# Kernel tuning notes

Measured on AMD Instinct MI355X. Metric: run time of the kernel, lower is better.

The kernel has to match this reference:

```python
import jax, jax.numpy as jnp
import numpy as np

G, N, H = 32, 128, 32
EDGE_ATTR_DIM = 16
NUM_SPATIAL = 512
NUM_EDGE_DIS = 128
MAX_DIST = 5
N_EDGES = 65536
N_PATHS = 1048576
N_LAYERS = 12


def setup_inputs() -> dict:
    key = jax.random.key(0)
    ks = jax.random.split(key, 8)
    rng = np.random.default_rng(0)
    attn_bias = jax.random.normal(ks[0], (G, N + 1, N + 1), jnp.float32)
    spatial_pos = jax.random.randint(ks[1], (G, N, N), 0, NUM_SPATIAL, jnp.int32)
    # unique (g,i,j) edge destinations -> deterministic scatter
    flat_e = rng.permutation(G * N * N)[:N_EDGES]
    g = flat_e // (N * N)
    rest = flat_e % (N * N)
    edge_index = jnp.asarray(np.stack([g, rest // N, rest % N]), jnp.int32)
    edge_attr = jax.random.normal(ks[2], (N_EDGES, EDGE_ATTR_DIM), jnp.float32)
    # unique (g,i,j,d) path destinations
    flat_p = rng.permutation(G * N * N * MAX_DIST)[:N_PATHS]
    pg = flat_p // (N * N * MAX_DIST)
    r = flat_p % (N * N * MAX_DIST)
    pi = r // (N * MAX_DIST)
    r = r % (N * MAX_DIST)
    pj = r // MAX_DIST
    pd = r % MAX_DIST
    src = rng.integers(0, N, N_PATHS)
    dst = rng.integers(0, N, N_PATHS)
    path_index = jnp.asarray(np.stack([pg, pi, pj, pd, src, dst]), jnp.int32)
    std = 0.02 / np.sqrt(N_LAYERS)
    edge_enc_w = jax.random.normal(ks[3], (H, EDGE_ATTR_DIM), jnp.float32) * std
    spatial_pos_emb = (jax.random.normal(ks[4], (NUM_SPATIAL, H), jnp.float32) * 0.02).at[0].set(0.0)  # padding_idx=0
    virt_dist = jax.random.normal(ks[5], (1, H), jnp.float32) * 0.02
    edge_dis_emb = jax.random.normal(ks[6], (NUM_EDGE_DIS * H * H, 1), jnp.float32) * 0.02
    return dict(attn_bias=attn_bias, spatial_pos=spatial_pos, edge_index=edge_index,
                edge_attr=edge_attr, path_index=path_index, edge_enc_w=edge_enc_w,
                spatial_pos_emb=spatial_pos_emb, virt_dist=virt_dist,
                edge_dis_emb=edge_dis_emb, max_dist=MAX_DIST)


def reference(attn_bias, spatial_pos, edge_index, edge_attr, path_index,
              edge_enc_w, spatial_pos_emb, virt_dist, edge_dis_emb, max_dist):
    n_graph, n1, _ = attn_bias.shape
    n_node = n1 - 1
    num_heads = edge_enc_w.shape[0]
    # [G, H, N+1, N+1] base bias (repeat over heads)
    gab = jnp.broadcast_to(attn_bias[:, None], (n_graph, num_heads, n1, n1))
    # spatial position bias: embedding lookup [G,N,N,H] -> [G,H,N,N]
    spb = jnp.transpose(spatial_pos_emb[spatial_pos], (0, 3, 1, 2))
    gab = gab.at[:, :, 1:, 1:].add(spb)
    t = virt_dist.reshape(1, num_heads, 1)
    gab = gab.at[:, :, 1:, 0].add(t)
    gab = gab.at[:, :, 0, :].add(t)
    # edge encoder: [E, edge_attr_dim] @ [edge_attr_dim, H] -> [E, H]
    ea = edge_attr @ edge_enc_w.T
    dense_adj = jnp.zeros((n_graph, n_node, n_node, num_heads), ea.dtype)
    dense_adj = dense_adj.at[edge_index[0], edge_index[1], edge_index[2]].set(ea)
    # multi-hop path features: scatter gathered edges into [G,N,N,D,H]
    edge_input = jnp.zeros((n_graph, n_node, n_node, max_dist, num_heads), ea.dtype)
    gathered = dense_adj[path_index[0], path_index[4], path_index[5]]
    edge_input = edge_input.at[path_index[0], path_index[1], path_index[2], path_index[3]].set(gathered)
    # path length normalizer
    sp = jnp.where(spatial_pos == 0, 1, spatial_pos)
    sp = jnp.where(sp > 1, sp - 1, sp)
    sp = jnp.clip(sp, 0, max_dist)
    # per-distance head mixing: [D, G*N*N, H] x [D, H, H]
    flat = jnp.transpose(edge_input, (3, 0, 1, 2, 4)).reshape(max_dist, -1, num_heads)
    W = edge_dis_emb.reshape(-1, num_heads, num_heads)[:max_dist]
    flat = jnp.einsum('dnh,dhk->dnk', flat, W)
    ei = flat.reshape(max_dist, n_graph, n_node, n_node, num_heads).transpose(1, 2, 3, 0, 4)
    ei = (ei.sum(-2) / sp[..., None].astype(ei.dtype)).transpose(0, 3, 1, 2)
    gab = gab.at[:, :, 1:, 1:].add(ei)
    return gab + attn_bias[:, None]
```

## Files before the change

### kernel.cpp

```cpp
#include <hip/hip_runtime.h>

#define G_    32
#define N_    128
#define NP1_  129
#define H_    32
#define EAD_  16
#define MAXD_ 5
#define NE_   65536
#define NPTH_ 1048576
#define PPB_  1024

__global__ __launch_bounds__(256) void edge_encode_kernel(
    const float* __restrict__ edge_attr,
    const int*   __restrict__ edge_index,
    const float* __restrict__ edge_enc_w,
    float*       __restrict__ eaval,
    int*         __restrict__ edge_map) {
  int t = blockIdx.x * blockDim.x + threadIdx.x;
  if (t >= NE_ * H_) return;
  int e = t >> 5;
  int h = t & 31;
  const float* ea = edge_attr + e * EAD_;
  const float* w  = edge_enc_w + h * EAD_;
  float s = 0.f;
#pragma unroll
  for (int k = 0; k < EAD_; ++k) s += ea[k] * w[k];
  eaval[t] = s;
  if (h == 0) {
    int g = edge_index[e];
    int i = edge_index[NE_ + e];
    int j = edge_index[2 * NE_ + e];
    edge_map[(g * N_ + i) * N_ + j] = e + 1;
  }
}

__global__ __launch_bounds__(256) void path_fused_kernel(
    const int*   __restrict__ path_index,
    const int*   __restrict__ edge_map,
    const float* __restrict__ eaval,
    const float* __restrict__ Wdis,
    float*       __restrict__ acc) {
  __shared__ int q_p[PPB_];
  __shared__ int q_e[PPB_];
  __shared__ int q_cnt;
  int tid = threadIdx.x;
  if (tid == 0) q_cnt = 0;
  __syncthreads();

  int base = blockIdx.x * PPB_;
#pragma unroll
  for (int k = 0; k < PPB_; k += 256) {
    int p = base + k + tid;
    int pg = path_index[p];
    int ps = path_index[4 * NPTH_ + p];
    int pt = path_index[5 * NPTH_ + p];
    int m = edge_map[(pg * N_ + ps) * N_ + pt];
    if (m) {
      int idx = atomicAdd(&q_cnt, 1);
      q_p[idx] = p;
      q_e[idx] = m - 1;
    }
  }
  __syncthreads();
  int cnt = q_cnt;

  int lane = tid & 31;
  int grp  = tid & 32;
  for (int s = tid >> 5; s < cnt; s += 8) {
    int p = q_p[s];
    int e = q_e[s];
    int pg = path_index[p];
    int pi = path_index[NPTH_ + p];
    int pj = path_index[2 * NPTH_ + p];
    int pd = path_index[3 * NPTH_ + p];
    float rv = eaval[e * H_ + lane];
    const float* Wd = Wdis + pd * H_ * H_;
    float v = 0.f;
#pragma unroll
    for (int h = 0; h < H_; ++h) {
      float rh = __shfl(rv, grp + h, 64);
      v += rh * Wd[h * H_ + lane];
    }
    atomicAdd(&acc[(((pg * N_) + pi) * N_ + pj) * H_ + lane], v);
  }
}

__global__ __launch_bounds__(256) void output_kernel(
    const float* __restrict__ attn_bias,
    const int*   __restrict__ spatial_pos,
    const float* __restrict__ spe,
    const float* __restrict__ virt,
    const float* __restrict__ acc,
    float*       __restrict__ out) {
  __shared__ float lds_val[N_ * 33];
  __shared__ float lds_virt[H_];

  int blk = blockIdx.x;
  int g = blk / NP1_;
  int a = blk - g * NP1_;
  int tid = threadIdx.x;

  if (tid < H_) lds_virt[tid] = virt[tid];

  const float* ab = attn_bias + (g * NP1_ + a) * NP1_;

  if (a == 0) {
    __syncthreads();
    for (int t = tid; t < H_ * NP1_; t += 256) {
      int h = t / NP1_;
      int b = t - h * NP1_;
      out[((g * H_ + h) * NP1_) * NP1_ + b] = 2.f * ab[b] + lds_virt[h];
    }
    return;
  }

  int i = a - 1;
  const float* acc_row = acc + ((g * N_ + i) * N_) * H_;
  const int*   sp_row  = spatial_pos + (g * N_ + i) * N_;

  for (int t = tid; t < N_ * H_; t += 256) {
    int j = t >> 5;
    int h = t & 31;
    int s = sp_row[j];
    int s2 = (s == 0) ? 1 : s;
    s2 = (s2 > 1) ? s2 - 1 : s2;
    s2 = (s2 > MAXD_) ? MAXD_ : s2;
    float inv = 1.0f / (float)s2;
    lds_val[j * 33 + h] = spe[s * H_ + h] + acc_row[t] * inv;
  }
  __syncthreads();

  for (int t = tid; t < H_ * NP1_; t += 256) {
    int h = t / NP1_;
    int b = t - h * NP1_;
    float val = 2.f * ab[b];
    if (b == 0) {
      val += lds_virt[h];
    } else {
      val += lds_val[(b - 1) * 33 + h];
    }
    out[((g * H_ + h) * NP1_ + a) * NP1_ + b] = val;
  }
}

extern "C" void kernel_launch(void* const* d_in, const int* in_sizes, int n_in,
                              void* d_out, int out_size, void* d_ws, size_t ws_size,
                              hipStream_t stream) {
  const float* attn_bias   = (const float*)d_in[0];
  const int*   spatial_pos = (const int*)d_in[1];
  const int*   edge_index  = (const int*)d_in[2];
  const float* edge_attr   = (const float*)d_in[3];
  const int*   path_index  = (const int*)d_in[4];
  const float* edge_enc_w  = (const float*)d_in[5];
  const float* spe         = (const float*)d_in[6];
  const float* virt        = (const float*)d_in[7];
  const float* edge_dis    = (const float*)d_in[8];
  float* out = (float*)d_out;

  const size_t ACC_ELEMS = (size_t)G_ * N_ * N_ * H_;
  const size_t MAP_ELEMS = (size_t)G_ * N_ * N_;

  float* acc      = (float*)d_ws;
  int*   edge_map = (int*)(acc + ACC_ELEMS);
  float* eaval    = (float*)(edge_map + MAP_ELEMS);

  hipMemsetAsync(acc, 0, (ACC_ELEMS + MAP_ELEMS) * sizeof(float), stream);

  {
    int total = NE_ * H_;
    edge_encode_kernel<<<(total + 255) / 256, 256, 0, stream>>>(
        edge_attr, edge_index, edge_enc_w, eaval, edge_map);
  }
  path_fused_kernel<<<NPTH_ / PPB_, 256, 0, stream>>>(
      path_index, edge_map, eaval, edge_dis, acc);
  output_kernel<<<G_ * NP1_, 256, 0, stream>>>(
      attn_bias, spatial_pos, spe, virt, acc, out);
}
```

Before: 105.8 us.

## Scatter path edge ids into slot table and fuse head-mixing into output kernel

Replaces the per-path head-mixing with float atomics into a 16M-element accumulator. The path kernel now records only the edge id per (g,i,j,d) slot. The output kernel then gathers up to five edge encodings per (i,j), does the 32x32 mixing in place and normalises it, with no atomics. This removes the large accumulator memset and the atomic traffic, at the cost of redundant reads of eaval and W inside the output kernel and more compute per output block.

```diff
diff --git a/kernel.cpp b/kernel.cpp
--- a/kernel.cpp
+++ b/kernel.cpp
@@ -8,7 +8,6 @@
 #define MAXD_ 5
 #define NE_   65536
 #define NPTH_ 1048576
-#define PPB_  1024
 
 __global__ __launch_bounds__(256) void edge_encode_kernel(
     const float* __restrict__ edge_attr,
@@ -34,63 +33,31 @@
   }
 }
 
-__global__ __launch_bounds__(256) void path_fused_kernel(
-    const int*   __restrict__ path_index,
-    const int*   __restrict__ edge_map,
-    const float* __restrict__ eaval,
-    const float* __restrict__ Wdis,
-    float*       __restrict__ acc) {
-  __shared__ int q_p[PPB_];
-  __shared__ int q_e[PPB_];
-  __shared__ int q_cnt;
-  int tid = threadIdx.x;
-  if (tid == 0) q_cnt = 0;
-  __syncthreads();
-
-  int base = blockIdx.x * PPB_;
-#pragma unroll
-  for (int k = 0; k < PPB_; k += 256) {
-    int p = base + k + tid;
-    int pg = path_index[p];
-    int ps = path_index[4 * NPTH_ + p];
-    int pt = path_index[5 * NPTH_ + p];
-    int m = edge_map[(pg * N_ + ps) * N_ + pt];
-    if (m) {
-      int idx = atomicAdd(&q_cnt, 1);
-      q_p[idx] = p;
-      q_e[idx] = m - 1;
-    }
-  }
-  __syncthreads();
-  int cnt = q_cnt;
-
-  int lane = tid & 31;
-  int grp  = tid & 32;
-  for (int s = tid >> 5; s < cnt; s += 8) {
-    int p = q_p[s];
-    int e = q_e[s];
-    int pg = path_index[p];
-    int pi = path_index[NPTH_ + p];
-    int pj = path_index[2 * NPTH_ + p];
-    int pd = path_index[3 * NPTH_ + p];
-    float rv = eaval[e * H_ + lane];
-    const float* Wd = Wdis + pd * H_ * H_;
-    float v = 0.f;
-#pragma unroll
-    for (int h = 0; h < H_; ++h) {
-      float rh = __shfl(rv, grp + h, 64);
-      v += rh * Wd[h * H_ + lane];
-    }
-    atomicAdd(&acc[(((pg * N_) + pi) * N_ + pj) * H_ + lane], v);
+__global__ __launch_bounds__(256) void path_scatter_kernel(
+    const int* __restrict__ path_index,
+    const int* __restrict__ edge_map,
+    int*       __restrict__ slot) {
+  int p = blockIdx.x * blockDim.x + threadIdx.x;
+  int pg = path_index[p];
+  int pi = path_index[NPTH_ + p];
+  int pj = path_index[2 * NPTH_ + p];
+  int pd = path_index[3 * NPTH_ + p];
+  int ps = path_index[4 * NPTH_ + p];
+  int pt = path_index[5 * NPTH_ + p];
+  int m = edge_map[(pg * N_ + ps) * N_ + pt];
+  if (m) {
+    slot[((pg * N_ + pi) * N_ + pj) * MAXD_ + pd] = m;
   }
 }
 
-__global__ __launch_bounds__(256) void output_kernel(
+__global__ __launch_bounds__(256) void output_fused_kernel(
     const float* __restrict__ attn_bias,
     const int*   __restrict__ spatial_pos,
     const float* __restrict__ spe,
     const float* __restrict__ virt,
-    const float* __restrict__ acc,
+    const int*   __restrict__ slot,
+    const float* __restrict__ eaval,
+    const float* __restrict__ Wdis,
     float*       __restrict__ out) {
   __shared__ float lds_val[N_ * 33];
   __shared__ float lds_virt[H_];
@@ -115,18 +82,43 @@
   }
 
   int i = a - 1;
-  const float* acc_row = acc + ((g * N_ + i) * N_) * H_;
-  const int*   sp_row  = spatial_pos + (g * N_ + i) * N_;
+  const int* sp_row   = spatial_pos + (g * N_ + i) * N_;
+  const int* slot_row = slot + (size_t)((g * N_ + i) * N_) * MAXD_;
 
-  for (int t = tid; t < N_ * H_; t += 256) {
-    int j = t >> 5;
-    int h = t & 31;
+  int grp  = tid >> 5;
+  int lane = tid & 31;
+
+#pragma unroll 1
+  for (int it = 0; it < 16; ++it) {
+    int j = grp * 16 + it;
+    const int* srow = slot_row + j * MAXD_;
+    float aacc = 0.f;
+#pragma unroll
+    for (int d = 0; d < MAXD_; ++d) {
+      int m = srow[d];
+      if (m) {
+        const float* ea = eaval + (size_t)(m - 1) * H_;
+        const float* Wd = Wdis + d * H_ * H_;
+        float v0 = 0.f, v1 = 0.f, v2 = 0.f, v3 = 0.f;
+#pragma unroll
+        for (int h = 0; h < H_; h += 4) {
+          v0 += ea[h + 0] * Wd[(h + 0) * H_ + lane];
+          v1 += ea[h + 1] * Wd[(h + 1) * H_ + lane];
+          v2 += ea[h + 2] * Wd[(h + 2) * H_ + lane];
+          v3 += ea[h + 3] * Wd[(h + 3) * H_ + lane];
+        }
+        aacc += (v0 + v1) + (v2 + v3);
+      }
+    }
     int s = sp_row[j];
     int s2 = (s == 0) ? 1 : s;
     s2 = (s2 > 1) ? s2 - 1 : s2;
     s2 = (s2 > MAXD_) ? MAXD_ : s2;
-    float inv = 1.0f / (float)s2;
-    lds_val[j * 33 + h] = spe[s * H_ + h] + acc_row[t] * inv;
+    float inv = (s2 == 1) ? 1.0f
+              : (s2 == 2) ? 0.5f
+              : (s2 == 3) ? (1.0f / 3.0f)
+              : (s2 == 4) ? 0.25f : 0.2f;
+    lds_val[j * 33 + lane] = spe[s * H_ + lane] + aacc * inv;
   }
   __syncthreads();
 
@@ -157,22 +149,22 @@
   const float* edge_dis    = (const float*)d_in[8];
   float* out = (float*)d_out;
 
-  const size_t ACC_ELEMS = (size_t)G_ * N_ * N_ * H_;
-  const size_t MAP_ELEMS = (size_t)G_ * N_ * N_;
+  const size_t SLOT_ELEMS = (size_t)G_ * N_ * N_ * MAXD_;
+  const size_t MAP_ELEMS  = (size_t)G_ * N_ * N_;
 
-  float* acc      = (float*)d_ws;
-  int*   edge_map = (int*)(acc + ACC_ELEMS);
+  int*   slot     = (int*)d_ws;
+  int*   edge_map = slot + SLOT_ELEMS;
   float* eaval    = (float*)(edge_map + MAP_ELEMS);
 
-  hipMemsetAsync(acc, 0, (ACC_ELEMS + MAP_ELEMS) * sizeof(float), stream);
+  hipMemsetAsync(slot, 0, (SLOT_ELEMS + MAP_ELEMS) * sizeof(int), stream);
 
   {
     int total = NE_ * H_;
     edge_encode_kernel<<<(total + 255) / 256, 256, 0, stream>>>(
         edge_attr, edge_index, edge_enc_w, eaval, edge_map);
   }
-  path_fused_kernel<<<NPTH_ / PPB_, 256, 0, stream>>>(
-      path_index, edge_map, eaval, edge_dis, acc);
-  output_kernel<<<G_ * NP1_, 256, 0, stream>>>(
-      attn_bias, spatial_pos, spe, virt, acc, out);
+  path_scatter_kernel<<<NPTH_ / 256, 256, 0, stream>>>(
+      path_index, edge_map, slot);
+  output_fused_kernel<<<G_ * NP1_, 256, 0, stream>>>(
+      attn_bias, spatial_pos, spe, virt, slot, eaval, edge_dis, out);
 }
```

Measured after the change: 179.3 us. +69.4%, slower.
